# Optimization experiments

Hardware: AMD Instinct MI355X
Metric: run time of the kernel (lower is better)

The kernel has to match this reference:

```python
import jax, jax.numpy as jnp
import numpy as np

D_MODEL = 512
N_HEADS = 8
D_K = D_MODEL // N_HEADS


def setup_inputs() -> dict:
    key = jax.random.key(0)
    ks = jax.random.split(key, 7)
    s = 1.0 / np.sqrt(D_MODEL)
    return {
        "x": jax.random.normal(ks[0], (2, 4096, D_MODEL), dtype=jnp.float32),
        "W_q": jax.random.normal(ks[1], (D_MODEL, D_MODEL), dtype=jnp.float32) * s,
        "W_k": jax.random.normal(ks[2], (D_MODEL, D_MODEL), dtype=jnp.float32) * s,
        "W_v": jax.random.normal(ks[3], (D_MODEL, D_MODEL), dtype=jnp.float32) * s,
        "b_v": jax.random.normal(ks[4], (D_MODEL,), dtype=jnp.float32) * s,
        "W_o": jax.random.normal(ks[5], (D_MODEL, D_MODEL), dtype=jnp.float32) * s,
        "b_o": jax.random.normal(ks[6], (D_MODEL,), dtype=jnp.float32) * s,
    }


def _split_heads(t):
    # [N, S, d_model] -> [N, H, S, d_k]
    N, S, _ = t.shape
    return t.reshape(N, S, N_HEADS, D_K).transpose(0, 2, 1, 3)


def reference(x, W_q, W_k, W_v, b_v, W_o, b_o):
    N, S, _ = x.shape
    # nn.Linear computes x @ W.T (+ b)
    Q = _split_heads(x @ W_q.T)
    K = _split_heads(x @ W_k.T)
    V = _split_heads(x @ W_v.T + b_v)
    scale = jnp.sqrt(jnp.asarray(D_K, x.dtype))
    scores = jnp.einsum('nhqd,nhkd->nhqk', Q, K) / scale  # [N,H,S,S]
    causal = jnp.tril(jnp.ones((S, S), dtype=bool))
    scores = jnp.where(causal, scores, -jnp.inf)
    attn = jax.nn.softmax(scores, axis=-1)
    out = jnp.einsum('nhqk,nhkd->nhqd', attn, V)  # [N,H,S,d_k]
    out = out.transpose(0, 2, 1, 3).reshape(N, S, D_MODEL)
    return out @ W_o.T + b_o
```

## Files before the change

### kernel.cpp

```cpp
#include <hip/hip_runtime.h>
#include <hip/hip_bf16.h>

#define NB 2
#define SEQ 4096
#define DM 512
#define NH 8
#define DKH 64
#define MTOT (NB*SEQ)

typedef __attribute__((ext_vector_type(4))) float f32x4;
typedef __attribute__((ext_vector_type(16))) float f32x16;
typedef __attribute__((ext_vector_type(8))) short bf16x8;
typedef __attribute__((ext_vector_type(2))) unsigned uint2v;

__device__ inline unsigned short f2bf(float f) {
    union { float f; unsigned int u; } v; v.f = f;
    unsigned int r = v.u + 0x7FFFu + ((v.u >> 16) & 1u);
    return (unsigned short)(r >> 16);
}

#define QSCALE 0.18033688011112042f

__global__ void cast_kernel(const float* __restrict__ x, const float* __restrict__ wq,
                            const float* __restrict__ wk, const float* __restrict__ wv,
                            const float* __restrict__ wo, unsigned short* __restrict__ dst) {
    const int NX = MTOT*DM;
    const int NW = DM*DM;
    int i4 = blockIdx.x * blockDim.x + threadIdx.x;
    long e = (long)i4 * 4;
    if (e >= NX + 4L*NW) return;
    const float* src; long off;
    if (e < NX)           { src = x;  off = e; }
    else if (e < NX+NW)   { src = wq; off = e - NX; }
    else if (e < NX+2*NW) { src = wk; off = e - NX - NW; }
    else if (e < NX+3*NW) { src = wv; off = e - NX - 2*NW; }
    else                  { src = wo; off = e - NX - 3*NW; }
    float4 v = *reinterpret_cast<const float4*>(src + off);
    ushort4 o;
    o.x = f2bf(v.x); o.y = f2bf(v.y); o.z = f2bf(v.z); o.w = f2bf(v.w);
    *reinterpret_cast<ushort4*>(dst + e) = o;
}

#define GEMM_KLOOP(BROW, BCOL)                                                     \
    f32x4 acc[4][4] = {};                                                          \
    for (int kt = 0; kt < 8; ++kt) {                                               \
        __syncthreads();                                                           \
        _Pragma("unroll")                                                          \
        for (int i = 0; i < 4; ++i) {                                              \
            int rbase = i*32 + wid*8;                                              \
            int row = rbase + (lane >> 3);                                         \
            int csrc = (lane & 7) ^ (row & 7);                                     \
            const unsigned short* asrc = Aptr_ + (long)((BROW)+row)*512 + kt*64 + csrc*8; \
            __builtin_amdgcn_global_load_lds(                                      \
                (const __attribute__((address_space(1))) unsigned int*)asrc,       \
                (__attribute__((address_space(3))) unsigned int*)&As[rbase*64], 16, 0, 0); \
            const unsigned short* bsrc = Bptr_ + (long)((BCOL)+row)*512 + kt*64 + csrc*8; \
            __builtin_amdgcn_global_load_lds(                                      \
                (const __attribute__((address_space(1))) unsigned int*)bsrc,       \
                (__attribute__((address_space(3))) unsigned int*)&Bs[rbase*64], 16, 0, 0); \
        }                                                                          \
        __syncthreads();                                                           \
        _Pragma("unroll")                                                          \
        for (int kk = 0; kk < 2; ++kk) {                                           \
            bf16x8 af[4], bfr[4];                                                  \
            _Pragma("unroll")                                                      \
            for (int mi = 0; mi < 4; ++mi) {                                       \
                int row = wr*64 + mi*16 + l15;                                     \
                int colb = (kk*32 + l4*8) * 2;                                     \
                af[mi] = *reinterpret_cast<const bf16x8*>(                         \
                    reinterpret_cast<const char*>(As) + row*128 + (colb ^ ((row&7)<<4))); \
            }                                                                      \
            _Pragma("unroll")                                                      \
            for (int ni = 0; ni < 4; ++ni) {                                       \
                int row = wc*64 + ni*16 + l15;                                     \
                int colb = (kk*32 + l4*8) * 2;                                     \
                bfr[ni] = *reinterpret_cast<const bf16x8*>(                        \
                    reinterpret_cast<const char*>(Bs) + row*128 + (colb ^ ((row&7)<<4))); \
            }                                                                      \
            _Pragma("unroll")                                                      \
            for (int mi = 0; mi < 4; ++mi)                                         \
                _Pragma("unroll")                                                  \
                for (int ni = 0; ni < 4; ++ni)                                     \
                    acc[mi][ni] = __builtin_amdgcn_mfma_f32_16x16x32_bf16(af[mi], bfr[ni], acc[mi][ni], 0, 0, 0); \
        }                                                                          \
    }

__global__ __launch_bounds__(256, 2) void gemm_qkv(
    const unsigned short* __restrict__ A,
    const unsigned short* __restrict__ B,
    const float* __restrict__ bv,
    unsigned short* __restrict__ Qh, unsigned short* __restrict__ Kh,
    unsigned short* __restrict__ Vt)
{
    __shared__ __align__(16) unsigned short As[128*64];
    __shared__ __align__(16) unsigned short Bs[128*64];
    __shared__ __align__(16) unsigned short Trs[64*136];
    int tid = threadIdx.x;
    int wid = tid >> 6, lane = tid & 63;
    int wr = wid >> 1, wc = wid & 1;
    int brow = blockIdx.x * 128;
    int by   = blockIdx.y;
    int bcol = by * 128;
    int l15 = lane & 15, l4 = lane >> 4;
    const unsigned short* Aptr_ = A;
    const unsigned short* Bptr_ = B;

    GEMM_KLOOP(brow, bcol)

    if (by < 8) {
        #pragma unroll
        for (int mi = 0; mi < 4; ++mi) {
            #pragma unroll
            for (int ni = 0; ni < 4; ++ni) {
                #pragma unroll
                for (int r = 0; r < 4; ++r) {
                    int row = brow + wr*64 + mi*16 + l4*4 + r;
                    int col = bcol + wc*64 + ni*16 + l15;
                    float v = acc[mi][ni][r];
                    int which = col >> 9;
                    int cw = col & 511;
                    int h = cw >> 6, d = cw & 63;
                    int b = row >> 12, s = row & 4095;
                    int bh = b*NH + h;
                    if (which == 0)
                        Qh[((long)(bh*SEQ + s))*DKH + d] = f2bf(v * QSCALE);
                    else
                        Kh[((long)(bh*SEQ + s))*DKH + d] = f2bf(v);
                }
            }
        }
    } else {
        const int b = brow >> 12;
        const int stile = brow & 4095;
        #pragma unroll 1
        for (int hs = 0; hs < 2; ++hs) {
            __syncthreads();
            if (wc == hs) {
                #pragma unroll
                for (int mi = 0; mi < 4; ++mi) {
                    #pragma unroll
                    for (int ni = 0; ni < 4; ++ni) {
                        #pragma unroll
                        for (int r = 0; r < 4; ++r) {
                            int rowLoc = wr*64 + mi*16 + l4*4 + r;
                            int colH = ni*16 + l15;
                            int cw = (bcol + hs*64 + colH) & 511;
                            Trs[colH*136 + rowLoc] = f2bf(acc[mi][ni][r] + bv[cw]);
                        }
                    }
                }
            }
            __syncthreads();
            #pragma unroll
            for (int pass = 0; pass < 4; ++pass) {
                int idx = pass*256 + tid;
                int dd = idx >> 4;
                int s8 = (idx & 15) << 3;
                bf16x8 vv = *reinterpret_cast<const bf16x8*>(&Trs[dd*136 + s8]);
                int cw = ((bcol - 1024) + hs*64 + dd);
                int h = cw >> 6, d = cw & 63;
                int bh = b*NH + h;
                *reinterpret_cast<bf16x8*>(Vt + ((long)(bh*DKH + d))*SEQ + stile + s8) = vv;
            }
        }
    }
}

__global__ __launch_bounds__(256, 2) void gemm_out(
    const unsigned short* __restrict__ A,
    const unsigned short* __restrict__ B,
    const float* __restrict__ bias, float* __restrict__ Cout)
{
    __shared__ __align__(16) unsigned short As[128*64];
    __shared__ __align__(16) unsigned short Bs[128*64];
    int tid = threadIdx.x;
    int wid = tid >> 6, lane = tid & 63;
    int wr = wid >> 1, wc = wid & 1;
    int brow = blockIdx.x * 128;
    int bcol = blockIdx.y * 128;
    int l15 = lane & 15, l4 = lane >> 4;
    const unsigned short* Aptr_ = A;
    const unsigned short* Bptr_ = B;

    GEMM_KLOOP(brow, bcol)

    #pragma unroll
    for (int mi = 0; mi < 4; ++mi) {
        #pragma unroll
        for (int ni = 0; ni < 4; ++ni) {
            #pragma unroll
            for (int r = 0; r < 4; ++r) {
                int row = brow + wr*64 + mi*16 + l4*4 + r;
                int col = bcol + wc*64 + ni*16 + l15;
                Cout[(long)row*DM + col] = acc[mi][ni][r] + bias[col];
            }
        }
    }
}

#define PV_STEP_M(SV, VLS, KS, B0, OD0, OD1, LS)  do {                             \
        unsigned c0, c1, c2, c3;                                                   \
        float t0 = SV[B0+0], t1 = SV[B0+1], t2 = SV[B0+2], t3 = SV[B0+3];          \
        float t4 = SV[B0+4], t5 = SV[B0+5], t6 = SV[B0+6], t7 = SV[B0+7];          \
        asm("v_cvt_pk_bf16_f32 %0, %1, %2" : "=v"(c0) : "v"(t0), "v"(t1));         \
        asm("v_cvt_pk_bf16_f32 %0, %1, %2" : "=v"(c1) : "v"(t2), "v"(t3));         \
        asm("v_cvt_pk_bf16_f32 %0, %1, %2" : "=v"(c2) : "v"(t4), "v"(t5));         \
        asm("v_cvt_pk_bf16_f32 %0, %1, %2" : "=v"(c3) : "v"(t6), "v"(t7));         \
        uint2v sw0 = __builtin_amdgcn_permlane32_swap(c0, c2, false, false);       \
        uint2v sw1 = __builtin_amdgcn_permlane32_swap(c1, c3, false, false);       \
        union { unsigned u[4]; bf16x8 v; } pu;                                     \
        pu.u[0] = sw0[0]; pu.u[1] = sw1[0]; pu.u[2] = sw0[1]; pu.u[3] = sw1[1];    \
        bf16x8 vf0 = *reinterpret_cast<const bf16x8*>(VLS + l31*128      + (((KS)*32 + hi*16) ^ swz)); \
        OD0 = __builtin_amdgcn_mfma_f32_32x32x16_bf16(vf0, pu.v, OD0, 0, 0, 0);    \
        bf16x8 vf1 = *reinterpret_cast<const bf16x8*>(VLS + (32+l31)*128 + (((KS)*32 + hi*16) ^ swz)); \
        OD1 = __builtin_amdgcn_mfma_f32_32x32x16_bf16(vf1, pu.v, OD1, 0, 0, 0);    \
        LS  = __builtin_amdgcn_mfma_f32_32x32x16_bf16(onesv, pu.v, LS, 0, 0, 0);   \
    } while (0)

__global__ __launch_bounds__(256, 3) void attn_fm(
    const unsigned short* __restrict__ Qh,
    const unsigned short* __restrict__ Kh,
    const unsigned short* __restrict__ Vt,
    unsigned short* __restrict__ Obf)
{
    __shared__ __align__(16) unsigned short Kc[3][64*64];
    __shared__ __align__(16) unsigned short Vc[3][64*64];
    const int tid = threadIdx.x;
    const int wid = tid >> 6, lane = tid & 63;
    const int g = wid & 1, p = wid >> 1;
    const int l31 = lane & 31;
    const int hi  = lane >> 5;

    const int id   = blockIdx.x;
    const int xcd  = id & 7;
    const int rest = id >> 3;
    const int bh   = xcd + ((rest & 1) << 3);
    const int t    = 63 - (rest >> 1);

    const unsigned short* Qbase = Qh + (long)bh*SEQ*DKH;
    const unsigned short* Kbase = Kh + (long)bh*SEQ*DKH;
    const unsigned short* Vbase = Vt + (long)bh*DKH*SEQ;

    const int q0w = t*64 + g*32;
    const int q   = q0w + l31;
    const int nu  = t + 1;
    const int swz = (l31 & 7) << 4;

    bf16x8 qf[4];
    #pragma unroll
    for (int kk = 0; kk < 4; ++kk)
        qf[kk] = *reinterpret_cast<const bf16x8*>(Qbase + (long)q*DKH + kk*16 + hi*8);

    bf16x8 onesv;
    #pragma unroll
    for (int e = 0; e < 8; ++e) onesv[e] = (short)0x3F80;

    auto STAGE = [&](int b, int key0) {
        #pragma unroll
        for (int ii = 0; ii < 2; ++ii) {
            const int rbase = wid*16 + ii*8;
            const int row = rbase + (lane >> 3);
            const int ck = (lane & 7) ^ (row & 7);
            const unsigned short* ksrc = Kbase + (long)(key0 + row)*DKH + ck*8;
            __builtin_amdgcn_global_load_lds(
                (const __attribute__((address_space(1))) unsigned int*)ksrc,
                (__attribute__((address_space(3))) unsigned int*)&Kc[b][rbase*64], 16, 0, 0);
            const unsigned short* vsrc = Vbase + (long)row*SEQ + key0 + ck*8;
            __builtin_amdgcn_global_load_lds(
                (const __attribute__((address_space(1))) unsigned int*)vsrc,
                (__attribute__((address_space(3))) unsigned int*)&Vc[b][rbase*64], 16, 0, 0);
        }
    };

    f32x16 od0 = {}, od1 = {}, ls = {};

    STAGE(0, 0);
    if (nu > 1) {
        STAGE(1, 64);
        asm volatile("s_waitcnt vmcnt(4)" ::: "memory");
    } else {
        asm volatile("s_waitcnt vmcnt(0)" ::: "memory");
    }
    __builtin_amdgcn_s_barrier();

    int bc = 0;
    #pragma unroll 1
    for (int u = 0; u < nu; ++u) {
        const int bn = (bc + 2 >= 3) ? bc - 1 : bc + 2;
        if (u + 2 < nu) STAGE(bn, (u + 2) << 6);

        const char* kl = reinterpret_cast<const char*>(&Kc[bc][0]) + p*32*128;
        const char* vl = reinterpret_cast<const char*>(&Vc[bc][0]);

        bf16x8 kfr[4];
        #pragma unroll
        for (int kk = 0; kk < 4; ++kk)
            kfr[kk] = *reinterpret_cast<const bf16x8*>(kl + l31*128 + ((kk*32 + hi*16) ^ swz));
        f32x16 sv = {};
        __builtin_amdgcn_s_setprio(1);
        #pragma unroll
        for (int kk = 0; kk < 4; ++kk)
            sv = __builtin_amdgcn_mfma_f32_32x32x16_bf16(kfr[kk], qf[kk], sv, 0, 0, 0);
        __builtin_amdgcn_s_setprio(0);

        if (u == t) {
            const int kbase = (u << 6) + (p << 5);
            #pragma unroll
            for (int r = 0; r < 16; ++r) {
                const int ko = (r&3) + 8*(r>>2) + 4*hi;
                if (kbase + ko > q) sv[r] = -1e30f;
            }
        }

        #pragma unroll
        for (int r = 0; r < 16; ++r)
            sv[r] = __builtin_amdgcn_exp2f(sv[r]);

        __builtin_amdgcn_s_setprio(1);
        PV_STEP_M(sv, vl, (2*p),     0, od0, od1, ls);
        PV_STEP_M(sv, vl, (2*p + 1), 8, od0, od1, ls);
        __builtin_amdgcn_s_setprio(0);

        if (u + 2 < nu) {
            asm volatile("s_waitcnt vmcnt(4)" ::: "memory");
        } else {
            asm volatile("s_waitcnt vmcnt(0)" ::: "memory");
        }
        __builtin_amdgcn_s_barrier();

        bc = (bc + 1 >= 3) ? 0 : bc + 1;
    }

    __syncthreads();
    float lsum = ls[0];
    char*  sod = reinterpret_cast<char*>(&Kc[g][0]);
    float* sml = reinterpret_cast<float*>(&Vc[g][0]);
    const int lswz = (lane & 7) << 4;
    if (p == 1) {
        #pragma unroll
        for (int i = 0; i < 4; ++i) {
            *reinterpret_cast<f32x4*>(sod + lane*128 + ((i*16) ^ lswz)) =
                (f32x4){od0[i*4+0], od0[i*4+1], od0[i*4+2], od0[i*4+3]};
            *reinterpret_cast<f32x4*>(sod + lane*128 + (((i+4)*16) ^ lswz)) =
                (f32x4){od1[i*4+0], od1[i*4+1], od1[i*4+2], od1[i*4+3]};
        }
        sml[lane] = lsum;
    }
    __syncthreads();
    if (p == 0) {
        lsum += sml[lane];
        #pragma unroll
        for (int i = 0; i < 4; ++i) {
            f32x4 t0 = *reinterpret_cast<const f32x4*>(sod + lane*128 + ((i*16) ^ lswz));
            f32x4 t1 = *reinterpret_cast<const f32x4*>(sod + lane*128 + (((i+4)*16) ^ lswz));
            #pragma unroll
            for (int k = 0; k < 4; ++k) {
                od0[i*4+k] += t0[k];
                od1[i*4+k] += t1[k];
            }
        }
        const float rls = 1.0f / lsum;
        const long obase = (long)((bh >> 3)*SEQ + q)*DM + (bh & 7)*DKH;
        #pragma unroll
        for (int rr = 0; rr < 4; ++rr) {
            ushort4 w0, w1;
            w0.x = f2bf(od0[rr*4+0]*rls); w0.y = f2bf(od0[rr*4+1]*rls);
            w0.z = f2bf(od0[rr*4+2]*rls); w0.w = f2bf(od0[rr*4+3]*rls);
            *reinterpret_cast<ushort4*>(Obf + obase + rr*8 + hi*4) = w0;
            w1.x = f2bf(od1[rr*4+0]*rls); w1.y = f2bf(od1[rr*4+1]*rls);
            w1.z = f2bf(od1[rr*4+2]*rls); w1.w = f2bf(od1[rr*4+3]*rls);
            *reinterpret_cast<ushort4*>(Obf + obase + 32 + rr*8 + hi*4) = w1;
        }
    }
}

extern "C" void kernel_launch(void* const* d_in, const int* in_sizes, int n_in,
                              void* d_out, int out_size, void* d_ws, size_t ws_size,
                              hipStream_t stream) {
    const float* x  = (const float*)d_in[0];
    const float* wq = (const float*)d_in[1];
    const float* wk = (const float*)d_in[2];
    const float* wv = (const float*)d_in[3];
    const float* bv = (const float*)d_in[4];
    const float* wo = (const float*)d_in[5];
    const float* bo = (const float*)d_in[6];
    float* out = (float*)d_out;

    unsigned short* ws = (unsigned short*)d_ws;
    unsigned short* Xbf  = ws;
    unsigned short* Wqkv = Xbf  + 4194304;
    unsigned short* Wob  = Wqkv + 786432;
    unsigned short* Qh   = Wob  + 262144;
    unsigned short* Kh   = Qh   + 4194304;
    unsigned short* Vt   = Kh   + 4194304;
    unsigned short* Obf  = Vt   + 4194304;

    cast_kernel<<<5120, 256, 0, stream>>>(x, wq, wk, wv, wo, Xbf);

    dim3 gqkv(64, 12);
    gemm_qkv<<<gqkv, 256, 0, stream>>>(Xbf, Wqkv, bv, Qh, Kh, Vt);

    attn_fm<<<1024, 256, 0, stream>>>(Qh, Kh, Vt, Obf);

    dim3 go(64, 4);
    gemm_out<<<go, 256, 0, stream>>>(Obf, Wob, bo, out);
}
```

Baseline: 102.1 us.

## Software-pipeline QK one tile ahead with double-buffered K/V and higher occupancy

The attention loop now computes the QK scores for the next key tile before the softmax and PV work on the current tile, so MFMA work overlaps the exp and PV stages. K is staged two tiles ahead and V one tile ahead, each in a two-slot LDS buffer instead of three. The smaller LDS footprint lets launch bounds ask for four blocks per CU instead of three. In exchange, per-iteration __syncthreads replaces the partial vmcnt waits, which may drain outstanding loads each iteration. Holding the extra score registers also raises register pressure.

New measurement: 120.0 us. +17.5%, slower.

```diff
diff --git a/kernel.cpp b/kernel.cpp
--- a/kernel.cpp
+++ b/kernel.cpp
@@ -217,14 +217,14 @@
         LS  = __builtin_amdgcn_mfma_f32_32x32x16_bf16(onesv, pu.v, LS, 0, 0, 0);   \
     } while (0)
 
-__global__ __launch_bounds__(256, 3) void attn_fm(
+__global__ __launch_bounds__(256, 4) void attn_fm(
     const unsigned short* __restrict__ Qh,
     const unsigned short* __restrict__ Kh,
     const unsigned short* __restrict__ Vt,
     unsigned short* __restrict__ Obf)
 {
-    __shared__ __align__(16) unsigned short Kc[3][64*64];
-    __shared__ __align__(16) unsigned short Vc[3][64*64];
+    __shared__ __align__(16) unsigned short Kc[2][64*64];
+    __shared__ __align__(16) unsigned short Vc[2][64*64];
     const int tid = threadIdx.x;
     const int wid = tid >> 6, lane = tid & 63;
     const int g = wid & 1, p = wid >> 1;
@@ -255,7 +255,7 @@
     #pragma unroll
     for (int e = 0; e < 8; ++e) onesv[e] = (short)0x3F80;
 
-    auto STAGE = [&](int b, int key0) {
+    auto STAGE_K = [&](int b, int key0) {
         #pragma unroll
         for (int ii = 0; ii < 2; ++ii) {
             const int rbase = wid*16 + ii*8;
@@ -265,43 +265,51 @@
             __builtin_amdgcn_global_load_lds(
                 (const __attribute__((address_space(1))) unsigned int*)ksrc,
                 (__attribute__((address_space(3))) unsigned int*)&Kc[b][rbase*64], 16, 0, 0);
+        }
+    };
+    auto STAGE_V = [&](int b, int key0) {
+        #pragma unroll
+        for (int ii = 0; ii < 2; ++ii) {
+            const int rbase = wid*16 + ii*8;
+            const int row = rbase + (lane >> 3);
+            const int ck = (lane & 7) ^ (row & 7);
             const unsigned short* vsrc = Vbase + (long)row*SEQ + key0 + ck*8;
             __builtin_amdgcn_global_load_lds(
                 (const __attribute__((address_space(1))) unsigned int*)vsrc,
                 (__attribute__((address_space(3))) unsigned int*)&Vc[b][rbase*64], 16, 0, 0);
         }
     };
+    auto QK = [&](int kb) -> f32x16 {
+        const char* kl = reinterpret_cast<const char*>(&Kc[kb][0]) + p*32*128;
+        bf16x8 kfr[4];
+        #pragma unroll
+        for (int kk = 0; kk < 4; ++kk)
+            kfr[kk] = *reinterpret_cast<const bf16x8*>(kl + l31*128 + ((kk*32 + hi*16) ^ swz));
+        f32x16 s = {};
+        __builtin_amdgcn_s_setprio(1);
+        #pragma unroll
+        for (int kk = 0; kk < 4; ++kk)
+            s = __builtin_amdgcn_mfma_f32_32x32x16_bf16(kfr[kk], qf[kk], s, 0, 0, 0);
+        __builtin_amdgcn_s_setprio(0);
+        return s;
+    };
 
     f32x16 od0 = {}, od1 = {}, ls = {};
 
-    STAGE(0, 0);
-    if (nu > 1) {
-        STAGE(1, 64);
-        asm volatile("s_waitcnt vmcnt(4)" ::: "memory");
-    } else {
-        asm volatile("s_waitcnt vmcnt(0)" ::: "memory");
-    }
-    __builtin_amdgcn_s_barrier();
-
-    int bc = 0;
+    STAGE_K(0, 0);
+    STAGE_V(0, 0);
+    if (nu > 1) STAGE_K(1, 64);
+    __syncthreads();
+    f32x16 sv = QK(0);
+    __syncthreads();
+
     #pragma unroll 1
     for (int u = 0; u < nu; ++u) {
-        const int bn = (bc + 2 >= 3) ? bc - 1 : bc + 2;
-        if (u + 2 < nu) STAGE(bn, (u + 2) << 6);
-
-        const char* kl = reinterpret_cast<const char*>(&Kc[bc][0]) + p*32*128;
-        const char* vl = reinterpret_cast<const char*>(&Vc[bc][0]);
-
-        bf16x8 kfr[4];
-        #pragma unroll
-        for (int kk = 0; kk < 4; ++kk)
-            kfr[kk] = *reinterpret_cast<const bf16x8*>(kl + l31*128 + ((kk*32 + hi*16) ^ swz));
-        f32x16 sv = {};
-        __builtin_amdgcn_s_setprio(1);
-        #pragma unroll
-        for (int kk = 0; kk < 4; ++kk)
-            sv = __builtin_amdgcn_mfma_f32_32x32x16_bf16(kfr[kk], qf[kk], sv, 0, 0, 0);
-        __builtin_amdgcn_s_setprio(0);
+        if (u + 2 < nu) STAGE_K(u & 1, (u + 2) << 6);
+        if (u + 1 < nu) STAGE_V((u + 1) & 1, (u + 1) << 6);
+
+        f32x16 svn = {};
+        if (u + 1 < nu) svn = QK((u + 1) & 1);
 
         if (u == t) {
             const int kbase = (u << 6) + (p << 5);
@@ -311,27 +319,20 @@
                 if (kbase + ko > q) sv[r] = -1e30f;
             }
         }
-
         #pragma unroll
         for (int r = 0; r < 16; ++r)
             sv[r] = __builtin_amdgcn_exp2f(sv[r]);
 
+        const char* vl = reinterpret_cast<const char*>(&Vc[u & 1][0]);
         __builtin_amdgcn_s_setprio(1);
         PV_STEP_M(sv, vl, (2*p),     0, od0, od1, ls);
         PV_STEP_M(sv, vl, (2*p + 1), 8, od0, od1, ls);
         __builtin_amdgcn_s_setprio(0);
 
-        if (u + 2 < nu) {
-            asm volatile("s_waitcnt vmcnt(4)" ::: "memory");
-        } else {
-            asm volatile("s_waitcnt vmcnt(0)" ::: "memory");
-        }
-        __builtin_amdgcn_s_barrier();
-
-        bc = (bc + 1 >= 3) ? 0 : bc + 1;
-    }
-
-    __syncthreads();
+        __syncthreads();
+        sv = svn;
+    }
+
     float lsum = ls[0];
     char*  sod = reinterpret_cast<char*>(&Kc[g][0]);
     float* sml = reinterpret_cast<float*>(&Vc[g][0]);
```
